# Kernel optimization log

Hardware: AMD Instinct MI355X
Metric: run time of the kernel (lower is better)

The kernel has to match this reference:

```python
import jax, jax.numpy as jnp
import numpy as np

N = 32768       # nodes
DEG = 8         # incoming edges per node (plus 1 self loop added by GCNConv)
HID = 128       # hidden_dim
WID = 128       # network_width (== hidden_dim, required by residual)
ND = 9          # SelfAttnAggregation.node_degree
AD = WID + ND   # attention embed dim = 137


def setup_inputs() -> dict:
    key = jax.random.key(0)
    ks = jax.random.split(key, 12)
    x = jax.random.normal(ks[0], (N, HID + 2), dtype=jnp.float32)
    # fixed in-degree graph: each node has DEG random incoming edges
    src = jax.random.randint(ks[1], (N * DEG,), 0, N, dtype=jnp.int32)
    dst = jnp.repeat(jnp.arange(N, dtype=jnp.int32), DEG)
    edge_index = jnp.stack([src, dst])
    s = 0.1
    return {
        "x": x,
        "edge_index": edge_index,
        "W1": jax.random.normal(ks[2], (HID + 2, WID), jnp.float32) * s,
        "b1": jax.random.normal(ks[3], (WID,), jnp.float32) * s,
        "W2": jax.random.normal(ks[4], (WID, WID), jnp.float32) * s,
        "b2": jax.random.normal(ks[5], (WID,), jnp.float32) * s,
        # [conv(2), attn(2), qkv(3), AD, AD] — torch MultiheadAttention in_proj
        "qkv_w": jax.random.normal(ks[6], (2, 2, 3, AD, AD), jnp.float32) * s,
        "qkv_b": jax.random.normal(ks[7], (2, 2, 3, AD), jnp.float32) * s,
        "out_w": jax.random.normal(ks[8], (2, 2, AD, AD), jnp.float32) * s,
        "out_b": jax.random.normal(ks[9], (2, 2, AD), jnp.float32) * s,
    }


def _mha(d, wqkv, bqkv, wo, bo):
    # d: [N, ND, AD]; single-head torch MultiheadAttention (q=k=v=d)
    q = jnp.einsum("nsd,ed->nse", d, wqkv[0]) + bqkv[0]
    k = jnp.einsum("nsd,ed->nse", d, wqkv[1]) + bqkv[1]
    v = jnp.einsum("nsd,ed->nse", d, wqkv[2]) + bqkv[2]
    scores = jnp.einsum("nqe,nke->nqk", q, k) / np.sqrt(AD).astype(np.float32)
    a = jax.nn.softmax(scores, axis=-1)
    o = jnp.einsum("nqk,nke->nqe", a, v)
    return jnp.einsum("nse,oe->nso", o, wo) + bo


def _gcn_attn_conv(h_in, W, b, neighbors, qkv_w, qkv_b, out_w, out_b):
    # GCNConv(normalize=False): lin -> gather messages -> SelfAttnAggregation -> +bias
    h = h_in @ W                                   # [N, WID]
    m = h[neighbors]                               # [N, ND, WID] irregular gather
    pos = jnp.broadcast_to(jnp.eye(ND, dtype=h.dtype), (N, ND, ND))
    d = jnp.concatenate([m, pos], axis=-1)         # [N, ND, AD]
    y = d + _mha(d, qkv_w[0], qkv_b[0], out_w[0], out_b[0]) \
          + _mha(d, qkv_w[1], qkv_b[1], out_w[1], out_b[1])
    return jnp.max(y[..., :WID], axis=1) + b       # [N, WID]


def _pairnorm(h):
    h = h - jnp.mean(h, axis=0, keepdims=True)
    denom = jnp.sqrt(1e-6 + jnp.mean(jnp.sum(h * h, axis=-1)))
    return h / denom


def reference(x, edge_index, W1, b1, W2, b2, qkv_w, qkv_b, out_w, out_b):
    src = edge_index[0]
    # [N, ND] neighbor table: DEG incoming sources + self loop (add_self_loops=True)
    nbr = jnp.concatenate(
        [src.reshape(N, DEG), jnp.arange(N, dtype=src.dtype)[:, None]], axis=1
    )
    u = _gcn_attn_conv(x, W1, b1, nbr, qkv_w[0], qkv_b[0], out_w[0], out_b[0])
    u = jax.nn.relu(_pairnorm(u))
    u = _gcn_attn_conv(u, W2, b2, nbr, qkv_w[1], qkv_b[1], out_w[1], out_b[1])
    u = jax.nn.relu(_pairnorm(u))
    x2 = x[:, :-2] + u                             # [N, HID]
    last = x2[:, -1]
    last = jnp.where((last > 1.0) | (last < -1.0), jnp.float32(0.0), last)
    return x2.at[:, -1].set(last) / 2.0
```

## Files before the change

kernel.cpp:

```cpp
#include <hip/hip_runtime.h>
#include <hip/hip_bf16.h>

#define NN 32768
#define DEG 8
#define PW 548
#define GW 676
#define SFW 420
#define TP 428

typedef unsigned short u16;
typedef unsigned int u32;

__device__ __forceinline__ float bf2f(u32 lo16) { return __uint_as_float(lo16 << 16); }

__global__ void detect_kernel(const void* __restrict__ x, int* __restrict__ flagp) {
  if (threadIdx.x == 0) {
    const u16* u = (const u16*)x;
    int insane = 0;
    for (int i = 0; i < 128; ++i) {
      int e = (u[i] >> 7) & 0xff;
      if (e == 0 || e == 0xff || e < 0x70 || e > 0x8f) insane++;
    }
    *flagp = (insane >= 16) ? 0 : 1;
  }
}

__global__ void cvt_kernel(const void* __restrict__ src, float* __restrict__ dst, int n,
                           const int* __restrict__ flagp) {
  const int f = *flagp;
  for (int i = blockIdx.x * 256 + threadIdx.x; i < n; i += gridDim.x * 256) {
    if (f) dst[i] = bf2f((u32)((const u16*)src)[i]);
    else   dst[i] = ((const float*)src)[i];
  }
}

__global__ __launch_bounds__(256) void derive_small_kernel(
    const float* __restrict__ qw, const float* __restrict__ qb,
    const float* __restrict__ ow, const float* __restrict__ ob,
    float* __restrict__ cq, float* __restrict__ ck, float* __restrict__ cvo,
    float* __restrict__ cc, float* __restrict__ bo_sum) {
  const int hd = blockIdx.x;
  const float* Wq = qw + (size_t)(hd*3 + 0) * 18769;
  const float* Wk = qw + (size_t)(hd*3 + 1) * 18769;
  const float* Wv = qw + (size_t)(hd*3 + 2) * 18769;
  const float* bq = qb + (hd*3 + 0) * 137;
  const float* bk = qb + (hd*3 + 1) * 137;
  const float* bv = qb + (hd*3 + 2) * 137;
  const float* Wo = ow + (size_t)hd * 18769;
  const int tid = threadIdx.x;

  for (int idx = tid; idx < 9*137; idx += 256) {
    int s = idx / 137, e = idx % 137;
    cq[hd*1233 + idx] = Wq[e*137 + 128 + s] + bq[e];
    ck[hd*1233 + idx] = Wk[e*137 + 128 + s] + bk[e];
  }
  __syncthreads();

  for (int idx = tid; idx < 9*128; idx += 256) {
    int s = idx >> 7, oi = idx & 127;
    float a = 0.f;
    for (int e = 0; e < 137; ++e) a += Wo[oi*137 + e] * (Wv[e*137 + 128 + s] + bv[e]);
    cvo[hd*1152 + idx] = a;
  }
  for (int idx = tid; idx < 81; idx += 256) {
    int i = idx / 9, j = idx % 9;
    float a = 0.f;
    for (int e = 0; e < 137; ++e) a += cq[hd*1233 + i*137 + e] * ck[hd*1233 + j*137 + e];
    cc[hd*81 + idx] = a;
  }
  if ((hd & 1) == 0) {
    int l = hd >> 1;
    for (int oi = tid; oi < 128; oi += 256)
      bo_sum[l*128 + oi] = ob[(l*2 + 0)*137 + oi] + ob[(l*2 + 1)*137 + oi];
  }
}

__global__ __launch_bounds__(256) void derive_mm_kernel(
    const float* __restrict__ qw, const float* __restrict__ ow,
    float* __restrict__ Mqk, float* __restrict__ Mvo) {
  const int hd = blockIdx.y;
  const float* Wq = qw + (size_t)(hd*3 + 0) * 18769;
  const float* Wk = qw + (size_t)(hd*3 + 1) * 18769;
  const float* Wv = qw + (size_t)(hd*3 + 2) * 18769;
  const float* Wo = ow + (size_t)hd * 18769;
  const int idx = blockIdx.x * 256 + threadIdx.x;
  const int row = idx >> 7, col = idx & 127;
  float sq = 0.f, so = 0.f;
  #pragma unroll 4
  for (int e = 0; e < 137; ++e) {
    sq += Wq[e*137 + row] * Wk[e*137 + col];
    so += Wo[row*137 + e] * Wv[e*137 + col];
  }
  Mqk[hd*16384 + idx] = sq;
  Mvo[hd*16384 + idx] = so;
}

__global__ void bigw_kernel(const float* __restrict__ qw,
                            const float* __restrict__ Mqk, const float* __restrict__ Mvo,
                            const float* __restrict__ cq, const float* __restrict__ ck,
                            float* __restrict__ BigW) {
  const int idx = blockIdx.x * 256 + threadIdx.x;
  if (idx >= 2 * 128 * PW) return;
  const int l = idx / (128 * PW);
  const int r = idx % (128 * PW);
  const int k = r / PW, col = r % PW;
  float v = 0.f;
  if (col < 128)       v = Mqk[(l*2 + 0)*16384 + k*128 + col];
  else if (col < 256)  v = Mqk[(l*2 + 1)*16384 + k*128 + (col - 128)];
  else if (col < 274) {
    int q = col - 256, t = q / 9, j = q % 9;
    const float* Wq = qw + (size_t)((l*2 + t)*3 + 0) * 18769;
    const float* ckp = ck + (l*2 + t)*1233 + j*137;
    float a = 0.f;
    for (int e = 0; e < 137; ++e) a += Wq[e*137 + k] * ckp[e];
    v = a;
  } else if (col < 292) {
    int q = col - 274, t = q / 9, i = q % 9;
    const float* Wk_ = qw + (size_t)((l*2 + t)*3 + 1) * 18769;
    const float* cqp = cq + (l*2 + t)*1233 + i*137;
    float a = 0.f;
    for (int e = 0; e < 137; ++e) a += cqp[e] * Wk_[e*137 + k];
    v = a;
  }
  else if (col < 420)  v = Mvo[(l*2 + 0)*16384 + (col - 292)*128 + k];
  else                 v = Mvo[(l*2 + 1)*16384 + (col - 420)*128 + k];
  BigW[idx] = v;
}

__global__ __launch_bounds__(256) void gemm128_kernel(
    const float* __restrict__ A, const float* __restrict__ B,
    float* __restrict__ C,
    int M, int K, int NC, int lda, int ldb, int ldc) {
  __shared__ float As[16][128];
  __shared__ float Bs[16][132];
  const int tid = threadIdx.x;
  const int row0 = blockIdx.y * 128, col0 = blockIdx.x * 128;
  const int tx = tid & 15, ty = tid >> 4;
  float acc[8][8] = {};
  const int nsteps = (K + 15) / 16;
  for (int step = 0; step < nsteps; ++step) {
    const int k0 = step * 16;
    {
      const int ar = tid >> 1, aq = (tid & 1) * 8;
      const float* Ap = A + (size_t)(row0 + ar) * lda + k0 + aq;
      float av[8];
      if (k0 + 16 <= K) {
        const float4 v0 = *(const float4*)Ap;
        const float4 v1 = *(const float4*)(Ap + 4);
        av[0]=v0.x; av[1]=v0.y; av[2]=v0.z; av[3]=v0.w;
        av[4]=v1.x; av[5]=v1.y; av[6]=v1.z; av[7]=v1.w;
      } else {
        #pragma unroll
        for (int p = 0; p < 8; ++p) av[p] = (k0 + aq + p < K) ? Ap[p] : 0.f;
      }
      #pragma unroll
      for (int p = 0; p < 8; ++p) As[aq + p][ar] = av[p];
    }
    {
      const int bk = tid >> 4, bc = (tid & 15) * 8;
      const int kg = k0 + bk;
      const float* Bp = B + (size_t)kg * ldb + col0 + bc;
      if (kg < K && col0 + bc + 8 <= NC) {
        *(float4*)&Bs[bk][bc]     = *(const float4*)Bp;
        *(float4*)&Bs[bk][bc + 4] = *(const float4*)(Bp + 4);
      } else {
        #pragma unroll
        for (int p = 0; p < 8; ++p)
          Bs[bk][bc + p] = (kg < K && col0 + bc + p < NC) ? Bp[p] : 0.f;
      }
    }
    __syncthreads();
    #pragma unroll
    for (int kk = 0; kk < 16; ++kk) {
      float a[8], b[8];
      *(float4*)&a[0] = *(const float4*)&As[kk][ty * 8];
      *(float4*)&a[4] = *(const float4*)&As[kk][ty * 8 + 4];
      *(float4*)&b[0] = *(const float4*)&Bs[kk][tx * 8];
      *(float4*)&b[4] = *(const float4*)&Bs[kk][tx * 8 + 4];
      #pragma unroll
      for (int i = 0; i < 8; ++i)
        #pragma unroll
        for (int j = 0; j < 8; ++j)
          acc[i][j] += a[i] * b[j];
    }
    __syncthreads();
  }
  #pragma unroll
  for (int i = 0; i < 8; ++i) {
    const int rr = row0 + ty * 8 + i;
    float* Cp = C + (size_t)rr * ldc + col0 + tx * 8;
    if (col0 + tx * 8 + 8 <= NC) {
      *(float4*)Cp       = make_float4(acc[i][0], acc[i][1], acc[i][2], acc[i][3]);
      *(float4*)(Cp + 4) = make_float4(acc[i][4], acc[i][5], acc[i][6], acc[i][7]);
    } else {
      #pragma unroll
      for (int j = 0; j < 8; ++j)
        if (col0 + tx * 8 + j < NC) Cp[j] = acc[i][j];
    }
  }
}

__global__ __launch_bounds__(256) void attn_kernel(
    const int* __restrict__ src, const float* __restrict__ G,
    const float* __restrict__ cvo, const float* __restrict__ cc,
    const float* __restrict__ bo_sum, const float* __restrict__ b_layer,
    int layer, float* __restrict__ res) {
  __shared__ float T[9][TP];
  __shared__ float As[2][9][9];
  __shared__ float ymax[2][128];
  __shared__ int nbr[9];
  const int n = blockIdx.x;
  const int tid = threadIdx.x;
  if (tid < 9) nbr[tid] = (tid < 8) ? src[n * DEG + tid] : n;
  __syncthreads();
  for (int it = tid; it < 9 * 105; it += 256) {
    const int s = it / 105, w = it % 105;
    *(float4*)&T[s][w * 4] = *(const float4*)(G + (size_t)nbr[s] * GW + w * 4);
  }
  __syncthreads();
  if (tid < 162) {
    const int t = tid / 81, r = tid % 81, i = r / 9, j = r % 9;
    const float* hm = &T[i][128 + t * 128];
    const float* hj = &T[j][0];
    float s = 0.f;
    #pragma unroll 8
    for (int c = 0; c < 128; c += 4) {
      const float4 a = *(const float4*)&hm[c];
      const float4 b = *(const float4*)&hj[c];
      s += a.x * b.x + a.y * b.y + a.z * b.z + a.w * b.w;
    }
    s += T[i][384 + t*9 + j] + T[j][402 + t*9 + i] + cc[(layer*2 + t)*81 + r];
    As[t][i][j] = s * 0.08543576577f;
  }
  __syncthreads();
  if (tid < 18) {
    const int t = tid / 9, i = tid % 9;
    float* row = &As[t][i][0];
    float m = -3e38f;
    #pragma unroll
    for (int j = 0; j < 9; ++j) m = fmaxf(m, row[j]);
    float ex[9], ssum = 0.f;
    #pragma unroll
    for (int j = 0; j < 9; ++j) { ex[j] = expf(row[j] - m); ssum += ex[j]; }
    const float inv = 1.f / ssum;
    #pragma unroll
    for (int j = 0; j < 9; ++j) row[j] = ex[j] * inv;
  }
  __syncthreads();
  {
    const int oi = tid & 127, half = tid >> 7;
    const float* cvo1 = cvo + (layer * 2 + 0) * 1152 + oi;
    const float* cvo2 = cvo + (layer * 2 + 1) * 1152 + oi;
    float vg1[9], vg2[9];
    #pragma unroll
    for (int j = 0; j < 9; ++j) {
      const float* gr = G + (size_t)nbr[j] * GW + oi;
      vg1[j] = gr[420] + cvo1[j * 128];
      vg2[j] = gr[548] + cvo2[j * 128];
    }
    float mx = -3e38f;
    const int i0 = half ? 5 : 0, i1 = half ? 9 : 5;
    for (int i = i0; i < i1; ++i) {
      float y = T[i][oi];
      #pragma unroll
      for (int j = 0; j < 9; ++j)
        y += As[0][i][j] * vg1[j] + As[1][i][j] * vg2[j];
      mx = fmaxf(mx, y);
    }
    ymax[half][oi] = mx;
  }
  __syncthreads();
  if (tid < 128) {
    const float v = fmaxf(ymax[0][tid], ymax[1][tid]) + bo_sum[layer*128 + tid] + b_layer[tid];
    res[(size_t)n * 128 + tid] = v;
  }
}

__global__ __launch_bounds__(256) void reduce_kernel(const float* __restrict__ res,
                                                     float* __restrict__ partial) {
  __shared__ float col2[128];
  __shared__ float sqs[256];
  const int b = blockIdx.x, tid = threadIdx.x;
  const int c = tid & 127, half = tid >> 7;
  float cs = 0.f, sq = 0.f;
  const int r0 = half * 64;
  for (int r = r0; r < r0 + 64; ++r) {
    const float v = res[((size_t)b * 128 + r) * 128 + c];
    cs += v; sq += v * v;
  }
  if (half) col2[c] = cs;
  sqs[tid] = sq;
  __syncthreads();
  if (!half) partial[b * 129 + c] = cs + col2[c];
  for (int s = 128; s >= 1; s >>= 1) {
    if (tid < s) sqs[tid] += sqs[tid + s];
    __syncthreads();
  }
  if (tid == 0) partial[b * 129 + 128] = sqs[0];
}

__global__ __launch_bounds__(128) void finalize_kernel(const float* __restrict__ partial,
                                                       float* __restrict__ stats) {
  __shared__ float musq[128];
  __shared__ float sqs[128];
  const int tid = threadIdx.x;
  float cs = 0.f;
  for (int b = 0; b < 256; ++b) cs += partial[b * 129 + tid];
  const float m = cs * (1.f / 32768.f);
  stats[tid] = m;
  musq[tid] = m * m;
  float sq = 0.f;
  for (int b = tid; b < 256; b += 128) sq += partial[b * 129 + 128];
  sqs[tid] = sq;
  __syncthreads();
  for (int s = 64; s >= 1; s >>= 1) {
    if (tid < s) { musq[tid] += musq[tid + s]; sqs[tid] += sqs[tid + s]; }
    __syncthreads();
  }
  if (tid == 0) {
    const float meansq = sqs[0] * (1.f / 32768.f);
    const float var = meansq - musq[0];
    stats[128] = 1.f / sqrtf(1e-6f + var);
  }
}

__global__ void norm_relu_kernel(const float* __restrict__ res, const float* __restrict__ stats,
                                 float* __restrict__ u) {
  const int idx = blockIdx.x * 256 + threadIdx.x;
  const int c = idx & 127;
  const float v = (res[idx] - stats[c]) * stats[128];
  u[idx] = fmaxf(v, 0.f);
}

__global__ void final_kernel(const float* __restrict__ res, const float* __restrict__ stats,
                             const float* __restrict__ xf, void* __restrict__ out,
                             const int* __restrict__ flagp) {
  const int idx = blockIdx.x * 256 + threadIdx.x;
  const int nrow = idx >> 7, c = idx & 127;
  float v = fmaxf((res[idx] - stats[c]) * stats[128], 0.f);
  v += xf[(size_t)nrow * 130 + c];
  if (c == 127 && (v > 1.f || v < -1.f)) v = 0.f;
  v *= 0.5f;
  if (*flagp) ((__hip_bfloat16*)out)[idx] = __float2bfloat16(v);
  else        ((float*)out)[idx] = v;
}

extern "C" void kernel_launch(void* const* d_in, const int* in_sizes, int n_in,
                              void* d_out, int out_size, void* d_ws, size_t ws_size,
                              hipStream_t stream) {
  (void)in_sizes; (void)n_in; (void)out_size; (void)ws_size;
  char* ws = (char*)d_ws;
  size_t off = 0;
  auto alloc = [&](size_t bytes) -> char* {
    char* p = ws + off;
    off += (bytes + 255) & ~(size_t)255;
    return p;
  };
  int*   flagp = (int*)  alloc(4);
  float* xf    = (float*)alloc((size_t)NN * 130 * 4);
  float* W1f   = (float*)alloc(130 * 128 * 4);
  float* b1f   = (float*)alloc(128 * 4);
  float* W2f   = (float*)alloc(128 * 128 * 4);
  float* b2f   = (float*)alloc(128 * 4);
  float* qwf   = (float*)alloc((size_t)225228 * 4);
  float* qbf   = (float*)alloc(1644 * 4);
  float* owf   = (float*)alloc((size_t)75076 * 4);
  float* obf   = (float*)alloc(548 * 4);
  float* Mqk   = (float*)alloc((size_t)4 * 16384 * 4);
  float* Mvo   = (float*)alloc((size_t)4 * 16384 * 4);
  float* cq    = (float*)alloc((size_t)4 * 1233 * 4);
  float* ck    = (float*)alloc((size_t)4 * 1233 * 4);
  float* cvo   = (float*)alloc((size_t)4 * 1152 * 4);
  float* cc    = (float*)alloc((size_t)4 * 81 * 4);
  float* boS   = (float*)alloc((size_t)2 * 128 * 4);
  float* BigW  = (float*)alloc((size_t)2 * 128 * PW * 4);
  float* G     = (float*)alloc((size_t)NN * GW * 4);
  float* res   = (float*)alloc((size_t)NN * 128 * 4);
  float* ubuf  = (float*)alloc((size_t)NN * 128 * 4);
  float* part  = (float*)alloc((size_t)256 * 129 * 4);
  float* st0   = (float*)alloc(132 * 4);
  float* st1   = (float*)alloc(132 * 4);

  const int* edge = (const int*)d_in[1];

  detect_kernel<<<1, 64, 0, stream>>>(d_in[0], flagp);

  struct CvtDesc { const void* src; float* dst; int n; };
  const CvtDesc cv[9] = {
    { d_in[0], xf,  NN * 130 },
    { d_in[2], W1f, 130 * 128 },
    { d_in[3], b1f, 128 },
    { d_in[4], W2f, 128 * 128 },
    { d_in[5], b2f, 128 },
    { d_in[6], qwf, 225228 },
    { d_in[7], qbf, 1644 },
    { d_in[8], owf, 75076 },
    { d_in[9], obf, 548 },
  };
  for (int i = 0; i < 9; ++i) {
    int blocks = (cv[i].n + 255) / 256;
    if (blocks > 4096) blocks = 4096;
    cvt_kernel<<<blocks, 256, 0, stream>>>(cv[i].src, cv[i].dst, cv[i].n, flagp);
  }

  derive_small_kernel<<<4, 256, 0, stream>>>(qwf, qbf, owf, obf, cq, ck, cvo, cc, boS);
  derive_mm_kernel<<<dim3(64, 4), 256, 0, stream>>>(qwf, owf, Mqk, Mvo);
  bigw_kernel<<<(2 * 128 * PW + 255) / 256, 256, 0, stream>>>(qwf, Mqk, Mvo, cq, ck, BigW);

  for (int l = 0; l < 2; ++l) {
    const float* act = l ? ubuf : xf;
    const int K = l ? 128 : 130;
    const float* W = l ? W2f : W1f;
    gemm128_kernel<<<dim3(1, NN / 128), 256, 0, stream>>>(
        act, W, G, NN, K, 128, K, 128, GW);
    gemm128_kernel<<<dim3((PW + 127) / 128, NN / 128), 256, 0, stream>>>(
        G, BigW + (size_t)l * 128 * PW, G + 128,
        NN, 128, PW, GW, PW, GW);
    attn_kernel<<<NN, 256, 0, stream>>>(edge, G, cvo, cc, boS,
                                        l ? b2f : b1f, l, res);
    reduce_kernel<<<256, 256, 0, stream>>>(res, part);
    finalize_kernel<<<1, 128, 0, stream>>>(part, l ? st1 : st0);
    if (l == 0) {
      norm_relu_kernel<<<NN * 128 / 256, 256, 0, stream>>>(res, st0, ubuf);
    } else {
      final_kernel<<<NN * 128 / 256, 256, 0, stream>>>(res, st1, xf, d_out, flagp);
    }
  }
}
```

Before: 743.1 us.

## Fold W into BigW, fuse pairnorm into GEMM, merge conversions, widen attention

```diff
diff --git a/kernel.cpp b/kernel.cpp
--- a/kernel.cpp
+++ b/kernel.cpp
@@ -5,7 +5,6 @@
 #define DEG 8
 #define PW 548
 #define GW 676
-#define SFW 420
 #define TP 428
 
 typedef unsigned short u16;
@@ -25,12 +24,22 @@
   }
 }
 
-__global__ void cvt_kernel(const void* __restrict__ src, float* __restrict__ dst, int n,
-                           const int* __restrict__ flagp) {
+struct CvtAll {
+  const void* src[9];
+  float* dst[9];
+  int cum[10];
+};
+
+__global__ void cvt_all_kernel(CvtAll d, const int* __restrict__ flagp) {
   const int f = *flagp;
-  for (int i = blockIdx.x * 256 + threadIdx.x; i < n; i += gridDim.x * 256) {
-    if (f) dst[i] = bf2f((u32)((const u16*)src)[i]);
-    else   dst[i] = ((const float*)src)[i];
+  const int total = d.cum[9];
+  for (int g = blockIdx.x * 256 + threadIdx.x; g < total; g += gridDim.x * 256) {
+    int s = 0;
+    #pragma unroll
+    for (int k = 1; k < 9; ++k) s += (g >= d.cum[k]);
+    const int i = g - d.cum[s];
+    if (f) d.dst[s][i] = bf2f((u32)((const u16*)d.src[s])[i]);
+    else   d.dst[s][i] = ((const float*)d.src[s])[i];
   }
 }
 
@@ -127,15 +136,41 @@
   BigW[idx] = v;
 }
 
+__global__ __launch_bounds__(256) void buildb_kernel(
+    const float* __restrict__ W1, const float* __restrict__ W2,
+    const float* __restrict__ BigW, float* __restrict__ BigB) {
+  const int l = blockIdx.y;
+  const int Kl = l ? 128 : 130;
+  const float* W = l ? W2 : W1;
+  const int idx = blockIdx.x * 256 + threadIdx.x;
+  if (idx >= Kl * 676) return;
+  const int k = idx / 676, c = idx % 676;
+  float v;
+  if (c < 128) {
+    v = W[k * 128 + c];
+  } else {
+    const int c2 = c - 128;
+    const float* Wk = W + k * 128;
+    const float* Bc = BigW + (size_t)l * 128 * PW + c2;
+    float a = 0.f;
+    #pragma unroll 4
+    for (int m = 0; m < 128; ++m) a += Wk[m] * Bc[(size_t)m * PW];
+    v = a;
+  }
+  BigB[(size_t)l * 130 * 676 + (size_t)k * 676 + c] = v;
+}
+
 __global__ __launch_bounds__(256) void gemm128_kernel(
     const float* __restrict__ A, const float* __restrict__ B,
     float* __restrict__ C,
-    int M, int K, int NC, int lda, int ldb, int ldc) {
+    int M, int K, int NC, int lda, int ldb, int ldc,
+    const float* __restrict__ astats) {
   __shared__ float As[16][128];
   __shared__ float Bs[16][132];
   const int tid = threadIdx.x;
   const int row0 = blockIdx.y * 128, col0 = blockIdx.x * 128;
   const int tx = tid & 15, ty = tid >> 4;
+  const float ainv = astats ? astats[128] : 1.f;
   float acc[8][8] = {};
   const int nsteps = (K + 15) / 16;
   for (int step = 0; step < nsteps; ++step) {
@@ -153,6 +188,13 @@
         #pragma unroll
         for (int p = 0; p < 8; ++p) av[p] = (k0 + aq + p < K) ? Ap[p] : 0.f;
       }
+      if (astats) {
+        #pragma unroll
+        for (int p = 0; p < 8; ++p) {
+          const int kc = k0 + aq + p;
+          if (kc < K) av[p] = fmaxf((av[p] - astats[kc]) * ainv, 0.f);
+        }
+      }
       #pragma unroll
       for (int p = 0; p < 8; ++p) As[aq + p][ar] = av[p];
     }
@@ -200,20 +242,21 @@
   }
 }
 
-__global__ __launch_bounds__(256) void attn_kernel(
+__global__ __launch_bounds__(512) void attn_kernel(
     const int* __restrict__ src, const float* __restrict__ G,
     const float* __restrict__ cvo, const float* __restrict__ cc,
     const float* __restrict__ bo_sum, const float* __restrict__ b_layer,
     int layer, float* __restrict__ res) {
   __shared__ float T[9][TP];
+  __shared__ float Gs[9][256];
   __shared__ float As[2][9][9];
-  __shared__ float ymax[2][128];
+  __shared__ float ymax[4][128];
   __shared__ int nbr[9];
   const int n = blockIdx.x;
   const int tid = threadIdx.x;
   if (tid < 9) nbr[tid] = (tid < 8) ? src[n * DEG + tid] : n;
   __syncthreads();
-  for (int it = tid; it < 9 * 105; it += 256) {
+  for (int it = tid; it < 9 * 105; it += 512) {
     const int s = it / 105, w = it % 105;
     *(float4*)&T[s][w * 4] = *(const float4*)(G + (size_t)nbr[s] * GW + w * 4);
   }
@@ -231,6 +274,11 @@
     }
     s += T[i][384 + t*9 + j] + T[j][402 + t*9 + i] + cc[(layer*2 + t)*81 + r];
     As[t][i][j] = s * 0.08543576577f;
+  } else if (tid >= 256) {
+    for (int it = tid - 256; it < 9 * 64; it += 256) {
+      const int s = it / 64, w = it % 64;
+      *(float4*)&Gs[s][w * 4] = *(const float4*)(G + (size_t)nbr[s] * GW + 420 + w * 4);
+    }
   }
   __syncthreads();
   if (tid < 18) {
@@ -248,30 +296,34 @@
   }
   __syncthreads();
   {
-    const int oi = tid & 127, half = tid >> 7;
+    const int oi = tid & 127, q = tid >> 7;
     const float* cvo1 = cvo + (layer * 2 + 0) * 1152 + oi;
     const float* cvo2 = cvo + (layer * 2 + 1) * 1152 + oi;
     float vg1[9], vg2[9];
     #pragma unroll
     for (int j = 0; j < 9; ++j) {
-      const float* gr = G + (size_t)nbr[j] * GW + oi;
-      vg1[j] = gr[420] + cvo1[j * 128];
-      vg2[j] = gr[548] + cvo2[j * 128];
+      vg1[j] = Gs[j][oi]       + cvo1[j * 128];
+      vg2[j] = Gs[j][128 + oi] + cvo2[j * 128];
     }
     float mx = -3e38f;
-    const int i0 = half ? 5 : 0, i1 = half ? 9 : 5;
-    for (int i = i0; i < i1; ++i) {
-      float y = T[i][oi];
-      #pragma unroll
-      for (int j = 0; j < 9; ++j)
-        y += As[0][i][j] * vg1[j] + As[1][i][j] * vg2[j];
-      mx = fmaxf(mx, y);
-    }
-    ymax[half][oi] = mx;
+    #pragma unroll
+    for (int ii = 0; ii < 3; ++ii) {
+      const int i = q + ii * 4;
+      if (i < 9) {
+        float y = T[i][oi];
+        #pragma unroll
+        for (int j = 0; j < 9; ++j)
+          y += As[0][i][j] * vg1[j] + As[1][i][j] * vg2[j];
+        mx = fmaxf(mx, y);
+      }
+    }
+    ymax[q][oi] = mx;
   }
   __syncthreads();
   if (tid < 128) {
-    const float v = fmaxf(ymax[0][tid], ymax[1][tid]) + bo_sum[layer*128 + tid] + b_layer[tid];
+    const float v = fmaxf(fmaxf(ymax[0][tid], ymax[1][tid]),
+                          fmaxf(ymax[2][tid], ymax[3][tid]))
+                  + bo_sum[layer*128 + tid] + b_layer[tid];
     res[(size_t)n * 128 + tid] = v;
   }
 }
@@ -299,37 +351,37 @@
   if (tid == 0) partial[b * 129 + 128] = sqs[0];
 }
 
-__global__ __launch_bounds__(128) void finalize_kernel(const float* __restrict__ partial,
-                                                       float* __restrict__ stats) {
+__global__ __launch_bounds__(1024) void finalize_kernel(const float* __restrict__ partial,
+                                                        float* __restrict__ stats) {
+  __shared__ float colsum[8][128];
+  __shared__ float sqred[256];
   __shared__ float musq[128];
-  __shared__ float sqs[128];
   const int tid = threadIdx.x;
+  const int c = tid & 127, g = tid >> 7;
   float cs = 0.f;
-  for (int b = 0; b < 256; ++b) cs += partial[b * 129 + tid];
-  const float m = cs * (1.f / 32768.f);
-  stats[tid] = m;
-  musq[tid] = m * m;
-  float sq = 0.f;
-  for (int b = tid; b < 256; b += 128) sq += partial[b * 129 + 128];
-  sqs[tid] = sq;
-  __syncthreads();
-  for (int s = 64; s >= 1; s >>= 1) {
-    if (tid < s) { musq[tid] += musq[tid + s]; sqs[tid] += sqs[tid + s]; }
+  #pragma unroll 8
+  for (int b = g * 32; b < g * 32 + 32; ++b) cs += partial[b * 129 + c];
+  colsum[g][c] = cs;
+  if (tid < 256) sqred[tid] = partial[tid * 129 + 128];
+  __syncthreads();
+  if (tid < 128) {
+    float m = 0.f;
+    #pragma unroll
+    for (int g2 = 0; g2 < 8; ++g2) m += colsum[g2][tid];
+    m *= (1.f / 32768.f);
+    stats[tid] = m;
+    musq[tid] = m * m;
+  }
+  __syncthreads();
+  for (int s = 128; s >= 1; s >>= 1) {
+    if (tid < s) sqred[tid] += sqred[tid + s];
+    if (s <= 64 && tid < s) musq[tid] += musq[tid + s];
     __syncthreads();
   }
   if (tid == 0) {
-    const float meansq = sqs[0] * (1.f / 32768.f);
-    const float var = meansq - musq[0];
+    const float var = sqred[0] * (1.f / 32768.f) - musq[0];
     stats[128] = 1.f / sqrtf(1e-6f + var);
   }
-}
-
-__global__ void norm_relu_kernel(const float* __restrict__ res, const float* __restrict__ stats,
-                                 float* __restrict__ u) {
-  const int idx = blockIdx.x * 256 + threadIdx.x;
-  const int c = idx & 127;
-  const float v = (res[idx] - stats[c]) * stats[128];
-  u[idx] = fmaxf(v, 0.f);
 }
 
 __global__ void final_kernel(const float* __restrict__ res, const float* __restrict__ stats,
@@ -374,9 +426,9 @@
   float* cc    = (float*)alloc((size_t)4 * 81 * 4);
   float* boS   = (float*)alloc((size_t)2 * 128 * 4);
   float* BigW  = (float*)alloc((size_t)2 * 128 * PW * 4);
+  float* BigB  = (float*)alloc((size_t)2 * 130 * 676 * 4);
   float* G     = (float*)alloc((size_t)NN * GW * 4);
   float* res   = (float*)alloc((size_t)NN * 128 * 4);
-  float* ubuf  = (float*)alloc((size_t)NN * 128 * 4);
   float* part  = (float*)alloc((size_t)256 * 129 * 4);
   float* st0   = (float*)alloc(132 * 4);
   float* st1   = (float*)alloc(132 * 4);
@@ -385,45 +437,38 @@
 
   detect_kernel<<<1, 64, 0, stream>>>(d_in[0], flagp);
 
-  struct CvtDesc { const void* src; float* dst; int n; };
-  const CvtDesc cv[9] = {
-    { d_in[0], xf,  NN * 130 },
-    { d_in[2], W1f, 130 * 128 },
-    { d_in[3], b1f, 128 },
-    { d_in[4], W2f, 128 * 128 },
-    { d_in[5], b2f, 128 },
-    { d_in[6], qwf, 225228 },
-    { d_in[7], qbf, 1644 },
-    { d_in[8], owf, 75076 },
-    { d_in[9], obf, 548 },
-  };
-  for (int i = 0; i < 9; ++i) {
-    int blocks = (cv[i].n + 255) / 256;
-    if (blocks > 4096) blocks = 4096;
-    cvt_kernel<<<blocks, 256, 0, stream>>>(cv[i].src, cv[i].dst, cv[i].n, flagp);
-  }
+  CvtAll ca;
+  {
+    const int srcidx[9] = {0, 2, 3, 4, 5, 6, 7, 8, 9};
+    float* dsts[9] = {xf, W1f, b1f, W2f, b2f, qwf, qbf, owf, obf};
+    const int ns[9] = {NN * 130, 130 * 128, 128, 128 * 128, 128,
+                       225228, 1644, 75076, 548};
+    int acc = 0;
+    for (int i = 0; i < 9; ++i) {
+      ca.src[i] = d_in[srcidx[i]];
+      ca.dst[i] = dsts[i];
+      ca.cum[i] = acc;
+      acc += ns[i];
+    }
+    ca.cum[9] = acc;
+  }
+  cvt_all_kernel<<<4096, 256, 0, stream>>>(ca, flagp);
 
   derive_small_kernel<<<4, 256, 0, stream>>>(qwf, qbf, owf, obf, cq, ck, cvo, cc, boS);
   derive_mm_kernel<<<dim3(64, 4), 256, 0, stream>>>(qwf, owf, Mqk, Mvo);
   bigw_kernel<<<(2 * 128 * PW + 255) / 256, 256, 0, stream>>>(qwf, Mqk, Mvo, cq, ck, BigW);
+  buildb_kernel<<<dim3((130 * 676 + 255) / 256, 2), 256, 0, stream>>>(W1f, W2f, BigW, BigB);
 
   for (int l = 0; l < 2; ++l) {
-    const float* act = l ? ubuf : xf;
+    const float* act = l ? res : xf;
     const int K = l ? 128 : 130;
-    const float* W = l ? W2f : W1f;
-    gemm128_kernel<<<dim3(1, NN / 128), 256, 0, stream>>>(
-        act, W, G, NN, K, 128, K, 128, GW);
-    gemm128_kernel<<<dim3((PW + 127) / 128, NN / 128), 256, 0, stream>>>(
-        G, BigW + (size_t)l * 128 * PW, G + 128,
-        NN, 128, PW, GW, PW, GW);
-    attn_kernel<<<NN, 256, 0, stream>>>(edge, G, cvo, cc, boS,
+    gemm128_kernel<<<dim3((GW + 127) / 128, NN / 128), 256, 0, stream>>>(
+        act, BigB + (size_t)l * 130 * 676, G,
+        NN, K, GW, K, 676, GW, l ? st0 : nullptr);
+    attn_kernel<<<NN, 512, 0, stream>>>(edge, G, cvo, cc, boS,
                                         l ? b2f : b1f, l, res);
     reduce_kernel<<<256, 256, 0, stream>>>(res, part);
-    finalize_kernel<<<1, 128, 0, stream>>>(part, l ? st1 : st0);
-    if (l == 0) {
-      norm_relu_kernel<<<NN * 128 / 256, 256, 0, stream>>>(res, st0, ubuf);
-    } else {
-      final_kernel<<<NN * 128 / 256, 256, 0, stream>>>(res, st1, xf, d_out, flagp);
-    }
-  }
-}
+    finalize_kernel<<<1, 1024, 0, stream>>>(part, l ? st1 : st0);
+  }
+  final_kernel<<<NN * 128 / 256, 256, 0, stream>>>(res, st1, xf, d_out, flagp);
+}
```

After: 850.7 us. +14.5%, slower.
